# Performance work log

Hardware: AMD Instinct MI355X
Metric: run time of the kernel (lower is better)

## Reference

```python
import jax, jax.numpy as jnp
import numpy as np


def setup_inputs() -> dict:
    key = jax.random.key(0)
    k1, k2, k3 = jax.random.split(key, 3)
    N, C, H, W = 2048, 512, 7, 7
    HW = H * W
    x = jax.random.normal(k1, (N, C, H, W), dtype=jnp.float32)
    attn = jax.random.uniform(k2, (N, HW, HW), dtype=jnp.float32)
    D = jax.random.normal(k3, (N, HW, C), dtype=jnp.float32)
    alpha = jnp.ones((1,), dtype=jnp.float32)
    return {"x": x, "attn": attn, "D": D, "alpha": alpha}


def reference(x, attn, D, alpha):
    # out[n,c,p] = alpha * sum_q attn[n,p,q] * D[n,q,c] + x[n,c,p]
    N, C, H, W = x.shape
    HW = H * W
    # attn @ D -> [N, HW, C], then move channel to front: [N, C, HW]
    y = jnp.einsum('npq,nqc->ncp', attn, D)  # fused bmm + transpose
    out = x + alpha[0] * y.reshape(N, C, H, W)
    return out
```

## Files before the change

### kernel.cpp

```cpp
#include <hip/hip_runtime.h>

#define N_BATCH 2048
#define HW 49
#define CCH 512
#define PADQ 52

typedef float f4 __attribute__((ext_vector_type(4)));

__global__ __launch_bounds__(256) void pad_attn(
    const float* __restrict__ attn, float* __restrict__ attnP)
{
    const int n = blockIdx.x;
    const int tid = threadIdx.x;
    const float* a = attn + (size_t)n * (HW * HW);
    float* t = attnP + (size_t)n * (HW * PADQ);
    for (int j = tid; j < HW * PADQ; j += 256) {
        const int p = j / PADQ;
        const int q = j - p * PADQ;
        t[j] = (q < HW) ? a[p * HW + q] : 0.0f;
    }
}

__global__ __launch_bounds__(256, 3) void fused_bmm_rowdot_add(
    const float* __restrict__ x, const float* __restrict__ D,
    const float* __restrict__ attnP, const float* __restrict__ alpha_p,
    float* __restrict__ out)
{
    __shared__ float ylds[256 * HW];
    const int bid = blockIdx.x;
    const int n   = bid >> 1;
    const int h   = bid & 1;
    const int tid = threadIdx.x;
    const int c   = h * 256 + tid;

    float d[PADQ];
    d[PADQ - 3] = 0.0f; d[PADQ - 2] = 0.0f; d[PADQ - 1] = 0.0f;
    const float* Dn = D + (size_t)n * (HW * CCH) + c;
    #pragma unroll
    for (int q = 0; q < HW; ++q) d[q] = Dn[(size_t)q * CCH];

    const f4* Af = (const f4*)(attnP + (size_t)n * (HW * PADQ));

    f4 aC[PADQ / 4];
    #pragma unroll
    for (int j = 0; j < PADQ / 4; ++j) aC[j] = Af[j];

    #pragma unroll 1
    for (int p = 0; p < HW; ++p) {
        const int pn = (p + 1 < HW) ? (p + 1) : p;
        f4 aN[PADQ / 4];
        #pragma unroll
        for (int j = 0; j < PADQ / 4; ++j) aN[j] = Af[pn * (PADQ / 4) + j];

        float s0 = 0.f, s1 = 0.f, s2 = 0.f, s3 = 0.f;
        #pragma unroll
        for (int j = 0; j < PADQ / 4; ++j) {
            s0 += aC[j].x * d[4 * j + 0];
            s1 += aC[j].y * d[4 * j + 1];
            s2 += aC[j].z * d[4 * j + 2];
            s3 += aC[j].w * d[4 * j + 3];
        }
        ylds[tid * HW + p] = (s0 + s1) + (s2 + s3);

        #pragma unroll
        for (int j = 0; j < PADQ / 4; ++j) aC[j] = aN[j];
    }

    __syncthreads();

    const float alpha = alpha_p[0];
    const size_t base = (size_t)n * (CCH * HW) + (size_t)h * (256 * HW);
    const f4* x4 = (const f4*)(x + base);
    f4*       o4 = (f4*)(out + base);
    const f4* y4 = (const f4*)ylds;
    for (int i = tid; i < (256 * HW) / 4; i += 256) {
        const f4 xv = x4[i];
        const f4 yv = y4[i];
        f4 ov = xv + alpha * yv;
        __builtin_nontemporal_store(ov, &o4[i]);
    }
}

extern "C" void kernel_launch(void* const* d_in, const int* in_sizes, int n_in,
                              void* d_out, int out_size, void* d_ws, size_t ws_size,
                              hipStream_t stream) {
    const float* x     = (const float*)d_in[0];
    const float* attn  = (const float*)d_in[1];
    const float* Dm    = (const float*)d_in[2];
    const float* alpha = (const float*)d_in[3];
    float* out = (float*)d_out;

    float* attnP = (float*)d_ws;

    pad_attn<<<N_BATCH, 256, 0, stream>>>(attn, attnP);
    fused_bmm_rowdot_add<<<N_BATCH * 2, 256, 0, stream>>>(x, Dm, attnP, alpha, out);
}
```

Measured before the change: 650.2 us.

## Fuse attn padding into main kernel via LDS staging and double-buffer rows

Removes the separate padding kernel and its workspace round trip. Each block now stages the padded attention matrix for its batch in shared memory, and threads read rows from LDS. The row loop is unrolled by two with explicit ping-pong register buffers. The extra LDS footprint lowers the occupancy bound from three to two blocks per CU.

After: 590.6 us. 9.2% less time.

```diff
diff --git a/kernel.cpp b/kernel.cpp
--- a/kernel.cpp
+++ b/kernel.cpp
@@ -7,31 +7,26 @@
 
 typedef float f4 __attribute__((ext_vector_type(4)));
 
-__global__ __launch_bounds__(256) void pad_attn(
-    const float* __restrict__ attn, float* __restrict__ attnP)
-{
-    const int n = blockIdx.x;
-    const int tid = threadIdx.x;
-    const float* a = attn + (size_t)n * (HW * HW);
-    float* t = attnP + (size_t)n * (HW * PADQ);
-    for (int j = tid; j < HW * PADQ; j += 256) {
-        const int p = j / PADQ;
-        const int q = j - p * PADQ;
-        t[j] = (q < HW) ? a[p * HW + q] : 0.0f;
-    }
-}
-
-__global__ __launch_bounds__(256, 3) void fused_bmm_rowdot_add(
+__global__ __launch_bounds__(256, 2) void fused_bmm_lds_bcast(
     const float* __restrict__ x, const float* __restrict__ D,
-    const float* __restrict__ attnP, const float* __restrict__ alpha_p,
+    const float* __restrict__ attn, const float* __restrict__ alpha_p,
     float* __restrict__ out)
 {
+    __shared__ float aT[HW * PADQ];
     __shared__ float ylds[256 * HW];
+
     const int bid = blockIdx.x;
     const int n   = bid >> 1;
     const int h   = bid & 1;
     const int tid = threadIdx.x;
     const int c   = h * 256 + tid;
+
+    const float* an = attn + (size_t)n * (HW * HW);
+    for (int j = tid; j < HW * PADQ; j += 256) {
+        const int r  = j / PADQ;
+        const int qq = j - r * PADQ;
+        aT[j] = (qq < HW) ? an[r * HW + qq] : 0.0f;
+    }
 
     float d[PADQ];
     d[PADQ - 3] = 0.0f; d[PADQ - 2] = 0.0f; d[PADQ - 1] = 0.0f;
@@ -39,32 +34,38 @@
     #pragma unroll
     for (int q = 0; q < HW; ++q) d[q] = Dn[(size_t)q * CCH];
 
-    const f4* Af = (const f4*)(attnP + (size_t)n * (HW * PADQ));
+    __syncthreads();
 
-    f4 aC[PADQ / 4];
+    const f4* Af = (const f4*)aT;
+
+#define DOT(BUF, PP)                                                  \
+    do {                                                              \
+        float s0 = 0.f, s1 = 0.f, s2 = 0.f, s3 = 0.f;                 \
+        _Pragma("unroll")                                             \
+        for (int j = 0; j < PADQ / 4; ++j) {                          \
+            s0 += BUF[j].x * d[4 * j + 0];                            \
+            s1 += BUF[j].y * d[4 * j + 1];                            \
+            s2 += BUF[j].z * d[4 * j + 2];                            \
+            s3 += BUF[j].w * d[4 * j + 3];                            \
+        }                                                             \
+        ylds[tid * HW + (PP)] = (s0 + s1) + (s2 + s3);                \
+    } while (0)
+
+    f4 Abuf[PADQ / 4], Bbuf[PADQ / 4];
     #pragma unroll
-    for (int j = 0; j < PADQ / 4; ++j) aC[j] = Af[j];
+    for (int j = 0; j < PADQ / 4; ++j) Abuf[j] = Af[j];
 
     #pragma unroll 1
-    for (int p = 0; p < HW; ++p) {
-        const int pn = (p + 1 < HW) ? (p + 1) : p;
-        f4 aN[PADQ / 4];
+    for (int p = 0; p < HW - 1; p += 2) {
         #pragma unroll
-        for (int j = 0; j < PADQ / 4; ++j) aN[j] = Af[pn * (PADQ / 4) + j];
-
-        float s0 = 0.f, s1 = 0.f, s2 = 0.f, s3 = 0.f;
+        for (int j = 0; j < PADQ / 4; ++j) Bbuf[j] = Af[(p + 1) * (PADQ / 4) + j];
+        DOT(Abuf, p);
         #pragma unroll
-        for (int j = 0; j < PADQ / 4; ++j) {
-            s0 += aC[j].x * d[4 * j + 0];
-            s1 += aC[j].y * d[4 * j + 1];
-            s2 += aC[j].z * d[4 * j + 2];
-            s3 += aC[j].w * d[4 * j + 3];
-        }
-        ylds[tid * HW + p] = (s0 + s1) + (s2 + s3);
-
-        #pragma unroll
-        for (int j = 0; j < PADQ / 4; ++j) aC[j] = aN[j];
+        for (int j = 0; j < PADQ / 4; ++j) Abuf[j] = Af[(p + 2) * (PADQ / 4) + j];
+        DOT(Bbuf, p + 1);
     }
+    DOT(Abuf, HW - 1);
+#undef DOT
 
     __syncthreads();
 
@@ -89,9 +90,7 @@
     const float* Dm    = (const float*)d_in[2];
     const float* alpha = (const float*)d_in[3];
     float* out = (float*)d_out;
+    (void)d_ws; (void)ws_size;
 
-    float* attnP = (float*)d_ws;
-
-    pad_attn<<<N_BATCH, 256, 0, stream>>>(attn, attnP);
-    fused_bmm_rowdot_add<<<N_BATCH * 2, 256, 0, stream>>>(x, Dm, attnP, alpha, out);
+    fused_bmm_lds_bcast<<<N_BATCH * 2, 256, 0, stream>>>(x, Dm, attn, alpha, out);
 }
```
